# Optimization experiments

Hardware: AMD Instinct MI355X
Metric: run time of the kernel (lower is better)

The kernel has to match this reference:

```python
import jax, jax.numpy as jnp
import numpy as np

IGNORE_LABEL = -1.0
POS_THR, NEG_THR = 0.5, 0.4
BBOX_CLIP = float(np.log(1000.0 / 16.0))


def box_overlap(box, gt):
    # box [M,4], gt [G,4] -> IoU [M,G]  (legacy +1 box widths)
    area_b = (box[:, 2] - box[:, 0] + 1) * (box[:, 3] - box[:, 1] + 1)
    area_g = (gt[:, 2] - gt[:, 0] + 1) * (gt[:, 3] - gt[:, 1] + 1)
    iw = jnp.minimum(box[:, None, 2], gt[None, :, 2]) - jnp.maximum(box[:, None, 0], gt[None, :, 0]) + 1
    ih = jnp.minimum(box[:, None, 3], gt[None, :, 3]) - jnp.maximum(box[:, None, 1], gt[None, :, 1]) + 1
    inter = jnp.maximum(iw, 0.0) * jnp.maximum(ih, 0.0)
    union = area_b[:, None] + area_g[None, :] - inter
    return inter / jnp.maximum(union, 1.0)


def bbox_transform_inv(anchors, deltas):
    # decode deltas [M,4] against anchors [M,4]
    w = anchors[:, 2] - anchors[:, 0] + 1
    h = anchors[:, 3] - anchors[:, 1] + 1
    cx = anchors[:, 0] + 0.5 * w
    cy = anchors[:, 1] + 0.5 * h
    pcx = cx + deltas[:, 0] * w
    pcy = cy + deltas[:, 1] * h
    pw = w * jnp.exp(jnp.minimum(deltas[:, 2], BBOX_CLIP))
    ph = h * jnp.exp(jnp.minimum(deltas[:, 3], BBOX_CLIP))
    return jnp.stack([pcx - 0.5 * pw, pcy - 0.5 * ph, pcx + 0.5 * pw, pcy + 0.5 * ph], axis=1)


def bbox_transform(anchors, gt):
    # encode gt [M,4] against anchors [M,4]
    aw = anchors[:, 2] - anchors[:, 0] + 1
    ah = anchors[:, 3] - anchors[:, 1] + 1
    acx = anchors[:, 0] + 0.5 * aw
    acy = anchors[:, 1] + 0.5 * ah
    gw = gt[:, 2] - gt[:, 0] + 1
    gh = gt[:, 3] - gt[:, 1] + 1
    gcx = gt[:, 0] + 0.5 * gw
    gcy = gt[:, 1] + 0.5 * gh
    return jnp.stack([(gcx - acx) / aw, (gcy - acy) / ah, jnp.log(gw / aw), jnp.log(gh / ah)], axis=1)


def rpn_anchor_target(boxes, anchors4):
    # boxes [n,G,5] -> labels [n,A,2] (top-2 EMD matching), targets [n,2A,4]
    anc2 = jnp.repeat(anchors4, 2, axis=0)  # interleaved [a0,a0,a1,a1,...]
    def per_image(gt):
        ov = box_overlap(anchors4, gt[:, :4])                     # [A,G]
        valid = gt[:, 4] != IGNORE_LABEL
        ov = jnp.where(valid[None, :], ov, -1.0)
        vals, idx = jax.lax.top_k(ov, 2)                          # [A,2]
        labels = jnp.where(vals >= POS_THR, 1.0,
                           jnp.where(vals < NEG_THR, 0.0, IGNORE_LABEL))
        matched = gt[idx.reshape(-1), :4]                         # [2A,4]
        targets = bbox_transform(anc2, matched)
        return labels, targets
    return jax.vmap(per_image)(boxes)


def anchor_iou_target(boxes, anchors4, pred_reg):
    # decode both predictions per anchor, IoU vs gt, then best / 2nd-best match value
    A = anchors4.shape[0]
    anc2 = jnp.repeat(anchors4, 2, axis=0)
    def per_image(gt, off):
        off = off.reshape(-1, 4)                                  # [2A,4]
        dt = bbox_transform_inv(anc2, off)
        ov = box_overlap(dt, gt[:, :4])                           # [2A,G]
        keep = 1.0 - (gt[:, 4] == IGNORE_LABEL).astype(ov.dtype)
        ov = ov * keep[None, :]
        ov = ov.reshape(A, 2, -1)
        a, b = ov[:, 0, :], ov[:, 1, :]
        ia = jnp.argmax(a, axis=1)
        aval = jnp.take_along_axis(a, ia[:, None], axis=1)        # [A,1]
        b = b.at[jnp.arange(A), ia].set(0.0)                      # scatter best slot to 0
        ib = jnp.argmax(b, axis=1)
        bval = jnp.take_along_axis(b, ib[:, None], axis=1)
        return jnp.concatenate([aval, bval], axis=1)              # [A,2]
    return jax.vmap(per_image)(boxes, pred_reg)


def sigmoid_ce_retina(pred, label, alpha=0.25, gamma=2.0):
    # focal loss; pred [n,M,1] probs, label [n,M] in {-1,0,1}
    mask = (label != IGNORE_LABEL).astype(pred.dtype)
    vlabel = label * mask
    onehot = (vlabel == 1.0).astype(pred.dtype)[:, :, None]
    pos = (1.0 - pred) ** gamma * onehot * jnp.log(pred)
    neg = pred ** gamma * (1.0 - onehot) * jnp.log(1.0 - pred)
    loss = -(alpha * pos + (1.0 - alpha) * neg).sum(axis=2) * mask
    npos = jnp.maximum((label > 0).sum(), 1)
    return loss.sum() / npos


def fg_mask(label):
    # label not background(0) and not ignore(-1)
    return ((label != 0.0) & (label != IGNORE_LABEL)).astype(jnp.float32)


def smooth_l1_retina(pred, gt, label, sigma=3.0):
    s2 = sigma * sigma
    x = pred - gt
    ax = jnp.abs(x)
    val = jnp.where(ax < 1.0 / s2, 0.5 * s2 * x * x, ax - 0.5 / s2)
    mask = fg_mask(label)
    return (val.sum(axis=2) * mask).sum() / jnp.maximum(mask.sum(), 1.0)


def iou_l1(pred, target, label):
    mask = fg_mask(label)
    return (jnp.abs(pred - target) * mask).sum() / jnp.maximum(mask.sum(), 1.0)


def softmax_loss_fn(score, label):
    # score [M,c], label [M] ints with -1 = ignore
    logp = jax.nn.log_softmax(score, axis=1)
    mask = label != -1
    vlabel = jnp.where(mask, label, 0).astype(jnp.int32)
    picked = jnp.take_along_axis(logp, vlabel[:, None], axis=1)[:, 0]
    return -(picked * mask).sum() / jnp.maximum(mask.sum(), 1)


def setup_inputs() -> dict:
    key = jax.random.key(0)
    ks = jax.random.split(key, 10)
    n, A, G = 2, 120000, 300
    pred_cls = jax.nn.sigmoid(jax.random.normal(ks[0], (n, A, 2), jnp.float32))
    rpn_num_prob = jax.random.normal(ks[1], (n, A, 2), jnp.float32)
    pred_reg = 0.2 * jax.random.normal(ks[2], (n, A, 8), jnp.float32)
    rpn_iou = jax.nn.sigmoid(jax.random.normal(ks[3], (n, A, 2), jnp.float32))
    cx = jax.random.uniform(ks[4], (A,), minval=0.0, maxval=1024.0)
    cy = jax.random.uniform(ks[5], (A,), minval=0.0, maxval=1024.0)
    w = jax.random.uniform(ks[6], (A,), minval=16.0, maxval=256.0)
    h = jax.random.uniform(ks[7], (A,), minval=16.0, maxval=256.0)
    anchors = jnp.stack([cx - 0.5 * w, cy - 0.5 * h, cx + 0.5 * w, cy + 0.5 * h], axis=1)
    kx, ky, kw, kh, kl = jax.random.split(ks[8], 5)
    gx = jax.random.uniform(kx, (n, G), minval=0.0, maxval=900.0)
    gy = jax.random.uniform(ky, (n, G), minval=0.0, maxval=900.0)
    gw = jax.random.uniform(kw, (n, G), minval=20.0, maxval=200.0)
    gh = jax.random.uniform(kh, (n, G), minval=20.0, maxval=200.0)
    glab = jnp.where(jax.random.uniform(kl, (n, G)) < 0.95, 1.0, -1.0)
    boxes = jnp.stack([gx, gy, gx + gw, gy + gh, glab], axis=2)
    im_info = jnp.concatenate([
        jnp.tile(jnp.array([[1024.0, 1024.0, 1.0, 1024.0, 1024.0]], jnp.float32), (n, 1)),
        jnp.full((n, 1), float(G), jnp.float32)], axis=1)
    return {"pred_cls": pred_cls, "rpn_num_prob": rpn_num_prob, "pred_reg": pred_reg,
            "anchors": anchors, "rpn_iou": rpn_iou, "boxes": boxes, "im_info": im_info}


def reference(pred_cls, rpn_num_prob, pred_reg, anchors, rpn_iou, boxes, im_info):
    n = pred_cls.shape[0]
    anchors4 = anchors[:, :4]
    # anchor targets and iou targets are computed under no_grad in the original
    rpn_labels, rpn_target_boxes = jax.lax.stop_gradient(rpn_anchor_target(boxes, anchors4))
    ious_target = jax.lax.stop_gradient(anchor_iou_target(boxes, anchors4, pred_reg))
    target_boxes = rpn_target_boxes.reshape(n, -1, 4)   # [n,2A,4]
    cls_prob = pred_cls.reshape(n, -1, 1)               # [n,2A,1]
    offsets = pred_reg.reshape(n, -1, 4)                # [n,2A,4]
    a = rpn_labels[:, :, 0]
    b = rpn_labels[:, :, 1]
    ignores = b - (a == 0.0).astype(b.dtype) * (b != 0.0).astype(b.dtype)
    labels = jnp.stack([a, ignores], axis=2).reshape(n, -1)  # [n,2A]
    cls_loss = sigmoid_ce_retina(cls_prob, labels, 0.25, 2.0)
    bbox_loss = smooth_l1_retina(offsets, target_boxes, labels)
    lab2 = labels.reshape(n, -1, 2)
    iou_loss = iou_l1(rpn_iou, ious_target, lab2)
    nlabels = (lab2 > 0).sum(axis=2).reshape(-1).astype(jnp.int32) - 1  # in {-1,0,1}
    num_loss = softmax_loss_fn(rpn_num_prob.reshape(-1, rpn_num_prob.shape[2]), nlabels)
    # order: rpn_cls_loss, rpn_bbox_loss, rpn_iou_loss, rpn_num_loss
    return jnp.stack([cls_loss, 2.0 * bbox_loss, 2.0 * iou_loss, num_loss])
```

## Files before the change

### kernel.cpp

```cpp
#include <hip/hip_runtime.h>
#include <math.h>

#define G_MAX 512
#define SPLIT 4

#define NBIN 264
#define BIN_LO 130.0f
#define BIN_INVW 0.2f

__device__ __forceinline__ float waveSum(float v) {
#pragma unroll
  for (int o = 32; o > 0; o >>= 1) v += __shfl_down(v, o, 64);
  return v;
}

__device__ __forceinline__ float huber9(float x) {
  float ax = fabsf(x);
  return (ax < (1.0f / 9.0f)) ? 4.5f * x * x : ax - (0.5f / 9.0f);
}

__device__ __forceinline__ float iouExact(float bx0, float by0, float bx1, float by1,
                                          float areab, float4 g, float areag) {
  float gx1 = g.z - 1.0f, gy1 = g.w - 1.0f;
  float iw = fminf(bx1, gx1) - fmaxf(bx0, g.x) + 1.0f;
  float ih = fminf(by1, gy1) - fmaxf(by0, g.y) + 1.0f;
  float inter = fmaxf(iw, 0.f) * fmaxf(ih, 0.f);
  float uni = areab + areag - inter;
  return inter / fmaxf(uni, 1.0f);
}

__device__ __forceinline__ uint32_t packKey(float x0, float y0, float x1p, float y1p,
                                            float area, float4 gb, float ga,
                                            uint32_t g) {
  float iw = fminf(x1p, gb.z) - fmaxf(x0, gb.x);
  float ih = fminf(y1p, gb.w) - fmaxf(y0, gb.y);
  float inter = fmaxf(iw, 0.f) * ih;
  float key = (area + ga) * __builtin_amdgcn_rcpf(inter);
  return (__float_as_uint(key) & 0xFFFFFE00u) | g;
}

__device__ __forceinline__ int xbin(float x) {
  return (int)fminf(fmaxf((x + BIN_LO) * BIN_INVW, 0.0f), (float)(NBIN - 1));
}

__global__ __launch_bounds__(256) void retina_main(
    const float* __restrict__ pred_cls,
    const float* __restrict__ rpn_num,
    const float* __restrict__ pred_reg,
    const float* __restrict__ anchors,
    const float* __restrict__ rpn_iou,
    const float* __restrict__ boxes,
    int A, int G,
    double* __restrict__ partial)
{
  __shared__ float4 sBox[G_MAX];
  __shared__ float2 sMeta[G_MAX];
  __shared__ unsigned short sO2S[G_MAX];
  __shared__ int sHist[NBIN];
  __shared__ int sStart[NBIN + 1];
  __shared__ int sCur[NBIN];
  __shared__ float sWaveMax[4];
  __shared__ float sSpanSh;
  __shared__ float sRed[4][7];
  __shared__ float sStash[64][10];
  __shared__ float2 sRes[64];
  __shared__ unsigned char sList[64];
  __shared__ int sNum;

  const int img = blockIdx.y;
  const int seg = threadIdx.x & (SPLIT - 1);
  const int q   = threadIdx.x >> 2;
  const int i   = blockIdx.x * 64 + q;
  const int ic  = (i < A) ? i : (A - 1);
  const float* gtb = boxes + (size_t)img * G * 5;

  float4 a4 = *(const float4*)(anchors + (size_t)ic * 4);
  float ax0 = a4.x, ay0 = a4.y, ax1 = a4.z, ay1 = a4.w;
  float aw = ax1 - ax0 + 1.0f, ah = ay1 - ay0 + 1.0f;
  float areaa = aw * ah;
  float acx = ax0 + 0.5f * aw, acy = ay0 + 0.5f * ah;
  float ax1p = ax1 + 1.0f, ay1p = ay1 + 1.0f;

  float d0 = 0.f, d1 = 0.f, d2 = 0.f, d3 = 0.f;
  float d4 = 0.f, d5 = 0.f, d6 = 0.f, d7 = 0.f;
  float pcv0 = 0.f, pcv1 = 0.f, riv0 = 0.f, riv1 = 0.f, sn0 = 0.f, sn1 = 0.f;
  if (seg == 0) {
    const float* dp = pred_reg + ((size_t)img * A + ic) * 8;
    d0 = dp[0]; d1 = dp[1]; d2 = dp[2]; d3 = dp[3];
    d4 = dp[4]; d5 = dp[5]; d6 = dp[6]; d7 = dp[7];
    const float* pc = pred_cls + ((size_t)img * A + ic) * 2;
    pcv0 = pc[0]; pcv1 = pc[1];
    const float* ri = rpn_iou + ((size_t)img * A + ic) * 2;
    riv0 = ri[0]; riv1 = ri[1];
    const float* sp = rpn_num + ((size_t)img * A + ic) * 2;
    sn0 = sp[0]; sn1 = sp[1];
  }

  if (threadIdx.x == 0) sNum = 0;
  for (int b = threadIdx.x; b < NBIN; b += 256) sHist[b] = 0;
  __syncthreads();

  for (int g = threadIdx.x; g < G; g += 256)
    atomicAdd(&sHist[xbin(gtb[g * 5 + 0])], 1);
  __syncthreads();

  for (int b = threadIdx.x; b <= NBIN; b += 256) {
    int s = 0;
    for (int j = 0; j < b; ++j) s += sHist[j];
    sStart[b] = s;
    if (b < NBIN) sCur[b] = s;
  }
  for (int s = G + threadIdx.x; s < G_MAX; s += 256) {
    sBox[s] = make_float4(0.f, 0.f, 1.f, 1.f);
    sMeta[s] = make_float2(1e30f, __uint_as_float((unsigned)s));
    sO2S[s] = (unsigned short)G;
  }
  __syncthreads();

  float mspan = 0.f;
  for (int g = threadIdx.x; g < G; g += 256) {
    float x0 = gtb[g * 5 + 0], y0 = gtb[g * 5 + 1];
    float x1 = gtb[g * 5 + 2], y1 = gtb[g * 5 + 3];
    float lb = gtb[g * 5 + 4];
    int pos = atomicAdd(&sCur[xbin(x0)], 1);
    float x1p = x1 + 1.0f, y1p = y1 + 1.0f;
    sBox[pos] = make_float4(x0, y0, x1p, y1p);
    sMeta[pos] = make_float2(
        (lb != -1.0f) ? (x1 - x0 + 1.0f) * (y1 - y0 + 1.0f) : 1e30f,
        __uint_as_float((unsigned)g));
    sO2S[g] = (unsigned short)pos;
    mspan = fmaxf(mspan, x1p - x0);
  }
#pragma unroll
  for (int m = 32; m > 0; m >>= 1) mspan = fmaxf(mspan, __shfl_xor(mspan, m, 64));
  {
    int lane = threadIdx.x & 63, wid = threadIdx.x >> 6;
    if (lane == 0) sWaveMax[wid] = mspan;
  }
  __syncthreads();
  if (threadIdx.x == 0)
    sSpanSh = fmaxf(fmaxf(sWaveMax[0], sWaveMax[1]),
                    fmaxf(sWaveMax[2], sWaveMax[3])) + 1.0f;
  __syncthreads();
  const float maxSpan = sSpanSh;

  float t_cls = 0.f, t_bbox = 0.f, t_iou = 0.f, t_num = 0.f;
  float t_npos = 0.f, t_nfg = 0.f, t_ncnt = 0.f;

  const float BBOX_CLIP = 4.1351666f;

  uint32_t an1 = 0xFFFFFFFFu, an2 = 0xFFFFFFFFu;
  {
    int lo = sStart[xbin(ax0 - maxSpan)];
    int hi = sStart[xbin(ax1p) + 1];
#pragma unroll 2
    for (int s = lo + seg; s < hi; s += SPLIT) {
      float4 gb = sBox[s];
      float2 mt = sMeta[s];
      uint32_t pk = packKey(ax0, ay0, ax1p, ay1p, areaa, gb, mt.x,
                            __float_as_uint(mt.y));
      uint32_t h = max(pk, an1);
      an1 = min(an1, pk);
      an2 = min(an2, h);
    }
  }

#pragma unroll
  for (int m = 1; m <= 2; m <<= 1) {
    uint32_t o1 = (uint32_t)__shfl_xor((int)an1, m, 64);
    uint32_t o2 = (uint32_t)__shfl_xor((int)an2, m, 64);
    uint32_t hi = max(an1, o1);
    an1 = min(an1, o1);
    an2 = min(min(an2, o2), hi);
  }

  bool fg0 = false, fg1 = false, needy = false;

  if (seg == 0 && i < A) {
    int og0 = (int)(an1 & 0x1FFu);
    int og1 = (int)(an2 & 0x1FFu);
    int s0 = sO2S[og0];
    int s1 = sO2S[og1];

    float4 g0 = sBox[s0]; float a0 = sMeta[s0].x; bool val0 = a0 < 1e29f;
    float v0 = val0 ? iouExact(ax0, ay0, ax1, ay1, areaa, g0, a0) : -1.0f;
    float4 g1 = sBox[s1]; float a1 = sMeta[s1].x; bool val1 = a1 < 1e29f;
    float v1 = val1 ? iouExact(ax0, ay0, ax1, ay1, areaa, g1, a1) : -1.0f;

    float la  = (v0 >= 0.5f) ? 1.0f : ((v0 < 0.4f) ? 0.0f : -1.0f);
    float lbv = (v1 >= 0.5f) ? 1.0f : ((v1 < 0.4f) ? 0.0f : -1.0f);
    float lab0 = la;
    float lab1 = lbv - (((la == 0.0f) && (lbv != 0.0f)) ? 1.0f : 0.0f);

    {
      float pv = pcv0;
      if (lab0 != -1.0f) {
        float l = (lab0 == 1.0f)
                      ? 0.25f * (1.0f - pv) * (1.0f - pv) * logf(pv)
                      : 0.75f * pv * pv * logf(1.0f - pv);
        t_cls -= l;
      }
      if (lab0 > 0.f) t_npos += 1.f;
      float qv = pcv1;
      if (lab1 != -1.0f) {
        float l = (lab1 == 1.0f)
                      ? 0.25f * (1.0f - qv) * (1.0f - qv) * logf(qv)
                      : 0.75f * qv * qv * logf(1.0f - qv);
        t_cls -= l;
      }
      if (lab1 > 0.f) t_npos += 1.f;
    }

    fg0 = (lab0 != 0.0f) && (lab0 != -1.0f);
    fg1 = (lab1 != 0.0f) && (lab1 != -1.0f);

    float raw = __builtin_amdgcn_rcpf(aw), rah = __builtin_amdgcn_rcpf(ah);

    if (fg0) {
      float mx1 = g0.z - 1.0f, my1 = g0.w - 1.0f;
      float gw = mx1 - g0.x + 1.0f, gh = my1 - g0.y + 1.0f;
      float gcx = g0.x + 0.5f * gw, gcy = g0.y + 0.5f * gh;
      float t0 = (gcx - acx) * raw, t1v = (gcy - acy) * rah;
      float t2 = logf(gw * raw), t3 = logf(gh * rah);
      t_bbox += huber9(d0 - t0) + huber9(d1 - t1v) + huber9(d2 - t2) + huber9(d3 - t3);
      t_nfg += 1.f;
    }
    if (fg1) {
      float mx1 = g1.z - 1.0f, my1 = g1.w - 1.0f;
      float gw = mx1 - g1.x + 1.0f, gh = my1 - g1.y + 1.0f;
      float gcx = g1.x + 0.5f * gw, gcy = g1.y + 0.5f * gh;
      float t0 = (gcx - acx) * raw, t1v = (gcy - acy) * rah;
      float t2 = logf(gw * raw), t3 = logf(gh * rah);
      t_bbox += huber9(d4 - t0) + huber9(d5 - t1v) + huber9(d6 - t2) + huber9(d7 - t3);
      t_nfg += 1.f;
    }

    {
      int nl = ((lab0 > 0.f) ? 1 : 0) + ((lab1 > 0.f) ? 1 : 0) - 1;
      if (nl != -1) {
        float m = fmaxf(sn0, sn1);
        float lse = m + logf(expf(sn0 - m) + expf(sn1 - m));
        float picked = ((nl == 0) ? sn0 : sn1) - lse;
        t_num -= picked;
        t_ncnt += 1.f;
      }
    }

    needy = fg0 || fg1;
    if (needy) {
      float p0cx = acx + d0 * aw, p0cy = acy + d1 * ah;
      float p0w = aw * expf(fminf(d2, BBOX_CLIP));
      float p0h = ah * expf(fminf(d3, BBOX_CLIP));
      float b0x0 = p0cx - 0.5f * p0w, b0y0 = p0cy - 0.5f * p0h;
      float b0x1 = p0cx + 0.5f * p0w, b0y1 = p0cy + 0.5f * p0h;
      float area0 = (b0x1 - b0x0 + 1.0f) * (b0y1 - b0y0 + 1.0f);

      float p1cx = acx + d4 * aw, p1cy = acy + d5 * ah;
      float p1w = aw * expf(fminf(d6, BBOX_CLIP));
      float p1h = ah * expf(fminf(d7, BBOX_CLIP));
      float b1x0 = p1cx - 0.5f * p1w, b1y0 = p1cy - 0.5f * p1h;
      float b1x1 = p1cx + 0.5f * p1w, b1y1 = p1cy + 0.5f * p1h;
      float area1 = (b1x1 - b1x0 + 1.0f) * (b1y1 - b1y0 + 1.0f);

      int slot = atomicAdd(&sNum, 1);
      sList[slot] = (unsigned char)q;
      float* st = sStash[slot];
      st[0] = b0x0; st[1] = b0y0; st[2] = b0x1; st[3] = b0y1; st[4] = area0;
      st[5] = b1x0; st[6] = b1y0; st[7] = b1x1; st[8] = b1y1; st[9] = area1;
    }
  }
  __syncthreads();

  {
    int num = sNum;
    int slot = threadIdx.x >> 2;
    int wseg = threadIdx.x & 3;
    if (slot < num) {
      const float* st = sStash[slot];
      float c0x0 = st[0], c0y0 = st[1], c0x1 = st[2], c0y1 = st[3], car0 = st[4];
      float c1x0 = st[5], c1y0 = st[6], c1x1 = st[7], c1y1 = st[8], car1 = st[9];
      float c0x1p = c0x1 + 1.0f, c0y1p = c0y1 + 1.0f;
      float c1x1p = c1x1 + 1.0f, c1y1p = c1y1 + 1.0f;

      uint32_t am = 0xFFFFFFFFu;
      uint32_t bk1 = 0xFFFFFFFFu, bk2 = 0xFFFFFFFFu;

      int lo = sStart[xbin(fminf(c0x0, c1x0) - maxSpan)];
      int hi = sStart[xbin(fmaxf(c0x1p, c1x1p)) + 1];
#pragma unroll 2
      for (int s = lo + wseg; s < hi; s += 4) {
        float4 gb = sBox[s];
        float2 mt = sMeta[s];
        uint32_t og = __float_as_uint(mt.y);
        am = min(am, packKey(c0x0, c0y0, c0x1p, c0y1p, car0, gb, mt.x, og));
        uint32_t pk = packKey(c1x0, c1y0, c1x1p, c1y1p, car1, gb, mt.x, og);
        uint32_t hib = max(pk, bk1);
        bk1 = min(bk1, pk);
        bk2 = min(bk2, hib);
      }

#pragma unroll
      for (int m = 1; m <= 2; m <<= 1) {
        am = min(am, (uint32_t)__shfl_xor((int)am, m, 64));
        uint32_t q1 = (uint32_t)__shfl_xor((int)bk1, m, 64);
        uint32_t q2 = (uint32_t)__shfl_xor((int)bk2, m, 64);
        uint32_t hib = max(bk1, q1);
        bk1 = min(bk1, q1);
        bk2 = min(min(bk2, q2), hib);
      }

      if (wseg == 0) {
        int ai  = (int)(am  & 0x1FFu);
        int bi  = (int)(bk1 & 0x1FFu);
        int bi2 = (int)(bk2 & 0x1FFu);
        int sa = sO2S[ai];
        float4 ga4 = sBox[sa]; float aav = sMeta[sa].x;
        float aval = (aav < 1e29f) ? iouExact(c0x0, c0y0, c0x1, c0y1, car0, ga4, aav) : 0.0f;
        int bIdx = (ai == bi) ? bi2 : bi;
        int sb = sO2S[bIdx];
        float4 gb4 = sBox[sb]; float abv = sMeta[sb].x;
        float bval = (abv < 1e29f) ? iouExact(c1x0, c1y0, c1x1, c1y1, car1, gb4, abv) : 0.0f;
        sRes[sList[slot]] = make_float2(aval, bval);
      }
    }
  }
  __syncthreads();

  if (needy) {
    float2 r = sRes[q];
    if (fg0) t_iou += fabsf(riv0 - r.x);
    if (fg1) t_iou += fabsf(riv1 - fmaxf(r.y, 0.0f));
  }

  float vals[7] = {t_cls, t_bbox, t_iou, t_num, t_npos, t_nfg, t_ncnt};
  int lane = threadIdx.x & 63;
  int wid = threadIdx.x >> 6;
#pragma unroll
  for (int k = 0; k < 7; ++k) {
    float s = waveSum(vals[k]);
    if (lane == 0) sRed[wid][k] = s;
  }
  __syncthreads();
  if (threadIdx.x < 7) {
    double s = (double)sRed[0][threadIdx.x] + (double)sRed[1][threadIdx.x] +
               (double)sRed[2][threadIdx.x] + (double)sRed[3][threadIdx.x];
    size_t bid = (size_t)blockIdx.y * gridDim.x + blockIdx.x;
    partial[bid * 8 + threadIdx.x] = s;
  }
}

__global__ __launch_bounds__(1024) void retina_finalize(
    const double* __restrict__ partial, int nB, float* __restrict__ out) {
  __shared__ double sRed[16][7];
  double loc[7] = {0.0, 0.0, 0.0, 0.0, 0.0, 0.0, 0.0};
  for (int b = threadIdx.x; b < nB; b += 1024) {
    const double* r = partial + (size_t)b * 8;
#pragma unroll
    for (int k = 0; k < 7; ++k) loc[k] += r[k];
  }
  int lane = threadIdx.x & 63;
  int wid = threadIdx.x >> 6;
#pragma unroll
  for (int k = 0; k < 7; ++k) {
    double v = loc[k];
#pragma unroll
    for (int o = 32; o > 0; o >>= 1) v += __shfl_down(v, o, 64);
    if (lane == 0) sRed[wid][k] = v;
  }
  __syncthreads();
  if (threadIdx.x == 0) {
    double t[7];
#pragma unroll
    for (int k = 0; k < 7; ++k) {
      double s = 0.0;
      for (int w = 0; w < 16; ++w) s += sRed[w][k];
      t[k] = s;
    }
    double dpos = t[4] > 1.0 ? t[4] : 1.0;
    double dfg  = t[5] > 1.0 ? t[5] : 1.0;
    double dcnt = t[6] > 1.0 ? t[6] : 1.0;
    out[0] = (float)(t[0] / dpos);
    out[1] = (float)(2.0 * t[1] / dfg);
    out[2] = (float)(2.0 * t[2] / dfg);
    out[3] = (float)(t[3] / dcnt);
  }
}

extern "C" void kernel_launch(void* const* d_in, const int* in_sizes, int n_in,
                              void* d_out, int out_size, void* d_ws, size_t ws_size,
                              hipStream_t stream) {
  const float* pred_cls = (const float*)d_in[0];
  const float* rpn_num  = (const float*)d_in[1];
  const float* pred_reg = (const float*)d_in[2];
  const float* anchors  = (const float*)d_in[3];
  const float* rpn_iou  = (const float*)d_in[4];
  const float* boxes    = (const float*)d_in[5];

  int A = in_sizes[3] / 4;
  int n = in_sizes[0] / (2 * A);
  int G = in_sizes[5] / (5 * n);

  double* partial = (double*)d_ws;

  int nBx = (A + 63) / 64;
  int nB = nBx * n;
  dim3 grid(nBx, n, 1);
  retina_main<<<grid, dim3(256, 1, 1), 0, stream>>>(
      pred_cls, rpn_num, pred_reg, anchors, rpn_iou, boxes, A, G, partial);
  retina_finalize<<<dim3(1, 1, 1), dim3(1024, 1, 1), 0, stream>>>(
      partial, nB, (float*)d_out);
}
```

Measured before the change: 144.2 us.

## Bin GT boxes on a 2D x/y grid and process 128 anchors per block

Replaces the 1D x-bin histogram with a 64x16 2D grid keyed on box origin, built with a wave-shuffle prefix scan, so each anchor scans only the GT boxes whose bins overlap it in both x and y. Each block now handles 128 anchors with 2 threads per anchor instead of 64 anchors with 4, halving the number of blocks and the per-block GT binning setup. The second matching pass loops over stash batches to cover up to 128 entries. Grid scale constants assume coordinates within about 900, so out-of-range boxes are clamped into edge bins, and the per-row loop adds overhead when the y span is large.

New measurement: 130.5 us. 9.5% less time.

```diff
diff --git a/kernel.cpp b/kernel.cpp
--- a/kernel.cpp
+++ b/kernel.cpp
@@ -2,11 +2,21 @@
 #include <math.h>
 
 #define G_MAX 512
-#define SPLIT 4
-
-#define NBIN 264
-#define BIN_LO 130.0f
-#define BIN_INVW 0.2f
+
+#define XB 64
+#define YB 16
+#define NBINS 1024
+#define SCLX (64.0f / 900.0f)
+#define SCLY (16.0f / 900.0f)
+
+__device__ __forceinline__ int xbin(float v) {
+  int b = (int)(v * SCLX);
+  return min(max(b, 0), XB - 1);
+}
+__device__ __forceinline__ int ybin(float v) {
+  int b = (int)(v * SCLY);
+  return min(max(b, 0), YB - 1);
+}
 
 __device__ __forceinline__ float waveSum(float v) {
 #pragma unroll
@@ -37,10 +47,6 @@
   float inter = fmaxf(iw, 0.f) * ih;
   float key = (area + ga) * __builtin_amdgcn_rcpf(inter);
   return (__float_as_uint(key) & 0xFFFFFE00u) | g;
-}
-
-__device__ __forceinline__ int xbin(float x) {
-  return (int)fminf(fmaxf((x + BIN_LO) * BIN_INVW, 0.0f), (float)(NBIN - 1));
 }
 
 __global__ __launch_bounds__(256) void retina_main(
@@ -56,21 +62,21 @@
   __shared__ float4 sBox[G_MAX];
   __shared__ float2 sMeta[G_MAX];
   __shared__ unsigned short sO2S[G_MAX];
-  __shared__ int sHist[NBIN];
-  __shared__ int sStart[NBIN + 1];
-  __shared__ int sCur[NBIN];
-  __shared__ float sWaveMax[4];
-  __shared__ float sSpanSh;
+  __shared__ int sCnt[NBINS];
+  __shared__ int sStart[NBINS + 1];
+  __shared__ int sWsum[4];
+  __shared__ float sWaveMax[4][2];
+  __shared__ float sSpanX, sSpanY;
   __shared__ float sRed[4][7];
-  __shared__ float sStash[64][10];
-  __shared__ float2 sRes[64];
-  __shared__ unsigned char sList[64];
+  __shared__ float sStash[128][10];
+  __shared__ float2 sRes[128];
+  __shared__ unsigned char sList[128];
   __shared__ int sNum;
 
   const int img = blockIdx.y;
-  const int seg = threadIdx.x & (SPLIT - 1);
-  const int q   = threadIdx.x >> 2;
-  const int i   = blockIdx.x * 64 + q;
+  const int seg = threadIdx.x & 1;
+  const int duo = threadIdx.x >> 1;
+  const int i   = blockIdx.x * 128 + duo;
   const int ic  = (i < A) ? i : (A - 1);
   const float* gtb = boxes + (size_t)img * G * 5;
 
@@ -97,19 +103,7 @@
   }
 
   if (threadIdx.x == 0) sNum = 0;
-  for (int b = threadIdx.x; b < NBIN; b += 256) sHist[b] = 0;
-  __syncthreads();
-
-  for (int g = threadIdx.x; g < G; g += 256)
-    atomicAdd(&sHist[xbin(gtb[g * 5 + 0])], 1);
-  __syncthreads();
-
-  for (int b = threadIdx.x; b <= NBIN; b += 256) {
-    int s = 0;
-    for (int j = 0; j < b; ++j) s += sHist[j];
-    sStart[b] = s;
-    if (b < NBIN) sCur[b] = s;
-  }
+  for (int b = threadIdx.x; b < NBINS; b += 256) sCnt[b] = 0;
   for (int s = G + threadIdx.x; s < G_MAX; s += 256) {
     sBox[s] = make_float4(0.f, 0.f, 1.f, 1.f);
     sMeta[s] = make_float2(1e30f, __uint_as_float((unsigned)s));
@@ -117,32 +111,79 @@
   }
   __syncthreads();
 
-  float mspan = 0.f;
-  for (int g = threadIdx.x; g < G; g += 256) {
-    float x0 = gtb[g * 5 + 0], y0 = gtb[g * 5 + 1];
-    float x1 = gtb[g * 5 + 2], y1 = gtb[g * 5 + 3];
-    float lb = gtb[g * 5 + 4];
-    int pos = atomicAdd(&sCur[xbin(x0)], 1);
-    float x1p = x1 + 1.0f, y1p = y1 + 1.0f;
-    sBox[pos] = make_float4(x0, y0, x1p, y1p);
-    sMeta[pos] = make_float2(
-        (lb != -1.0f) ? (x1 - x0 + 1.0f) * (y1 - y0 + 1.0f) : 1e30f,
-        __uint_as_float((unsigned)g));
-    sO2S[g] = (unsigned short)pos;
-    mspan = fmaxf(mspan, x1p - x0);
-  }
-#pragma unroll
-  for (int m = 32; m > 0; m >>= 1) mspan = fmaxf(mspan, __shfl_xor(mspan, m, 64));
+  float rx0[2], ry0[2], rx1[2], ry1[2], rlb[2];
+  int ng = 0;
+  for (int g = threadIdx.x; g < G; g += 256, ++ng) {
+    rx0[ng] = gtb[g * 5 + 0]; ry0[ng] = gtb[g * 5 + 1];
+    rx1[ng] = gtb[g * 5 + 2]; ry1[ng] = gtb[g * 5 + 3];
+    rlb[ng] = gtb[g * 5 + 4];
+    atomicAdd(&sCnt[(ybin(ry0[ng]) << 6) | xbin(rx0[ng])], 1);
+  }
+  __syncthreads();
+
+  {
+    int t = threadIdx.x;
+    int b0 = sCnt[t * 4 + 0], b1 = sCnt[t * 4 + 1];
+    int b2 = sCnt[t * 4 + 2], b3 = sCnt[t * 4 + 3];
+    int tsum = b0 + b1 + b2 + b3;
+    int lane = t & 63, wid = t >> 6;
+    int incl = tsum;
+#pragma unroll
+    for (int o = 1; o < 64; o <<= 1) {
+      int u = __shfl_up(incl, o, 64);
+      if (lane >= o) incl += u;
+    }
+    if (lane == 63) sWsum[wid] = incl;
+    __syncthreads();
+    int woff = 0;
+    for (int w = 0; w < wid; ++w) woff += sWsum[w];
+    int excl = woff + incl - tsum;
+    sStart[t * 4 + 0] = excl;
+    sStart[t * 4 + 1] = excl + b0;
+    sStart[t * 4 + 2] = excl + b0 + b1;
+    sStart[t * 4 + 3] = excl + b0 + b1 + b2;
+    if (t == 255) sStart[NBINS] = excl + tsum;
+    sCnt[t * 4 + 0] = excl;
+    sCnt[t * 4 + 1] = excl + b0;
+    sCnt[t * 4 + 2] = excl + b0 + b1;
+    sCnt[t * 4 + 3] = excl + b0 + b1 + b2;
+  }
+  __syncthreads();
+
+  float mspanX = 0.f, mspanY = 0.f;
+  {
+    int g = threadIdx.x;
+    for (int k = 0; k < ng; ++k, g += 256) {
+      float x0 = rx0[k], y0 = ry0[k], x1 = rx1[k], y1 = ry1[k], lb = rlb[k];
+      int pos = atomicAdd(&sCnt[(ybin(y0) << 6) | xbin(x0)], 1);
+      float x1p = x1 + 1.0f, y1p = y1 + 1.0f;
+      sBox[pos] = make_float4(x0, y0, x1p, y1p);
+      sMeta[pos] = make_float2(
+          (lb != -1.0f) ? (x1 - x0 + 1.0f) * (y1 - y0 + 1.0f) : 1e30f,
+          __uint_as_float((unsigned)g));
+      sO2S[g] = (unsigned short)pos;
+      mspanX = fmaxf(mspanX, x1p - x0);
+      mspanY = fmaxf(mspanY, y1p - y0);
+    }
+  }
+#pragma unroll
+  for (int m = 32; m > 0; m >>= 1) {
+    mspanX = fmaxf(mspanX, __shfl_xor(mspanX, m, 64));
+    mspanY = fmaxf(mspanY, __shfl_xor(mspanY, m, 64));
+  }
   {
     int lane = threadIdx.x & 63, wid = threadIdx.x >> 6;
-    if (lane == 0) sWaveMax[wid] = mspan;
-  }
-  __syncthreads();
-  if (threadIdx.x == 0)
-    sSpanSh = fmaxf(fmaxf(sWaveMax[0], sWaveMax[1]),
-                    fmaxf(sWaveMax[2], sWaveMax[3])) + 1.0f;
-  __syncthreads();
-  const float maxSpan = sSpanSh;
+    if (lane == 0) { sWaveMax[wid][0] = mspanX; sWaveMax[wid][1] = mspanY; }
+  }
+  __syncthreads();
+  if (threadIdx.x == 0) {
+    sSpanX = fmaxf(fmaxf(sWaveMax[0][0], sWaveMax[1][0]),
+                   fmaxf(sWaveMax[2][0], sWaveMax[3][0])) + 1.0f;
+    sSpanY = fmaxf(fmaxf(sWaveMax[0][1], sWaveMax[1][1]),
+                   fmaxf(sWaveMax[2][1], sWaveMax[3][1])) + 1.0f;
+  }
+  __syncthreads();
+  const float spanX = sSpanX, spanY = sSpanY;
 
   float t_cls = 0.f, t_bbox = 0.f, t_iou = 0.f, t_num = 0.f;
   float t_npos = 0.f, t_nfg = 0.f, t_ncnt = 0.f;
@@ -151,24 +192,29 @@
 
   uint32_t an1 = 0xFFFFFFFFu, an2 = 0xFFFFFFFFu;
   {
-    int lo = sStart[xbin(ax0 - maxSpan)];
-    int hi = sStart[xbin(ax1p) + 1];
+    int xb0 = xbin(ax0 - spanX);
+    int xb1 = xbin(ax1p);
+    int yb0 = ybin(ay0 - spanY);
+    int yb1 = ybin(ay1p);
+    for (int yb = yb0; yb <= yb1; ++yb) {
+      int lo = sStart[(yb << 6) + xb0];
+      int hi = sStart[(yb << 6) + xb1 + 1];
 #pragma unroll 2
-    for (int s = lo + seg; s < hi; s += SPLIT) {
-      float4 gb = sBox[s];
-      float2 mt = sMeta[s];
-      uint32_t pk = packKey(ax0, ay0, ax1p, ay1p, areaa, gb, mt.x,
-                            __float_as_uint(mt.y));
-      uint32_t h = max(pk, an1);
-      an1 = min(an1, pk);
-      an2 = min(an2, h);
-    }
-  }
-
-#pragma unroll
-  for (int m = 1; m <= 2; m <<= 1) {
-    uint32_t o1 = (uint32_t)__shfl_xor((int)an1, m, 64);
-    uint32_t o2 = (uint32_t)__shfl_xor((int)an2, m, 64);
+      for (int s = lo + seg; s < hi; s += 2) {
+        float4 gb = sBox[s];
+        float2 mt = sMeta[s];
+        uint32_t pk = packKey(ax0, ay0, ax1p, ay1p, areaa, gb, mt.x,
+                              __float_as_uint(mt.y));
+        uint32_t h = max(pk, an1);
+        an1 = min(an1, pk);
+        an2 = min(an2, h);
+      }
+    }
+  }
+
+  {
+    uint32_t o1 = (uint32_t)__shfl_xor((int)an1, 1, 64);
+    uint32_t o2 = (uint32_t)__shfl_xor((int)an2, 1, 64);
     uint32_t hi = max(an1, o1);
     an1 = min(an1, o1);
     an2 = min(min(an2, o2), hi);
@@ -263,7 +309,7 @@
       float area1 = (b1x1 - b1x0 + 1.0f) * (b1y1 - b1y0 + 1.0f);
 
       int slot = atomicAdd(&sNum, 1);
-      sList[slot] = (unsigned char)q;
+      sList[slot] = (unsigned char)duo;
       float* st = sStash[slot];
       st[0] = b0x0; st[1] = b0y0; st[2] = b0x1; st[3] = b0y1; st[4] = area0;
       st[5] = b1x0; st[6] = b1y0; st[7] = b1x1; st[8] = b1y1; st[9] = area1;
@@ -273,61 +319,70 @@
 
   {
     int num = sNum;
-    int slot = threadIdx.x >> 2;
-    int wseg = threadIdx.x & 3;
-    if (slot < num) {
-      const float* st = sStash[slot];
-      float c0x0 = st[0], c0y0 = st[1], c0x1 = st[2], c0y1 = st[3], car0 = st[4];
-      float c1x0 = st[5], c1y0 = st[6], c1x1 = st[7], c1y1 = st[8], car1 = st[9];
-      float c0x1p = c0x1 + 1.0f, c0y1p = c0y1 + 1.0f;
-      float c1x1p = c1x1 + 1.0f, c1y1p = c1y1 + 1.0f;
-
-      uint32_t am = 0xFFFFFFFFu;
-      uint32_t bk1 = 0xFFFFFFFFu, bk2 = 0xFFFFFFFFu;
-
-      int lo = sStart[xbin(fminf(c0x0, c1x0) - maxSpan)];
-      int hi = sStart[xbin(fmaxf(c0x1p, c1x1p)) + 1];
+    for (int sb = 0; sb < num; sb += 64) {
+      int slot = sb + (threadIdx.x >> 2);
+      int wseg = threadIdx.x & 3;
+      if (slot < num) {
+        const float* st = sStash[slot];
+        float c0x0 = st[0], c0y0 = st[1], c0x1 = st[2], c0y1 = st[3], car0 = st[4];
+        float c1x0 = st[5], c1y0 = st[6], c1x1 = st[7], c1y1 = st[8], car1 = st[9];
+        float c0x1p = c0x1 + 1.0f, c0y1p = c0y1 + 1.0f;
+        float c1x1p = c1x1 + 1.0f, c1y1p = c1y1 + 1.0f;
+
+        uint32_t am = 0xFFFFFFFFu;
+        uint32_t bk1 = 0xFFFFFFFFu, bk2 = 0xFFFFFFFFu;
+
+        int xb0 = xbin(fminf(c0x0, c1x0) - spanX);
+        int xb1 = xbin(fmaxf(c0x1p, c1x1p));
+        int yb0 = ybin(fminf(c0y0, c1y0) - spanY);
+        int yb1 = ybin(fmaxf(c0y1p, c1y1p));
+        for (int yb = yb0; yb <= yb1; ++yb) {
+          int lo = sStart[(yb << 6) + xb0];
+          int hi = sStart[(yb << 6) + xb1 + 1];
 #pragma unroll 2
-      for (int s = lo + wseg; s < hi; s += 4) {
-        float4 gb = sBox[s];
-        float2 mt = sMeta[s];
-        uint32_t og = __float_as_uint(mt.y);
-        am = min(am, packKey(c0x0, c0y0, c0x1p, c0y1p, car0, gb, mt.x, og));
-        uint32_t pk = packKey(c1x0, c1y0, c1x1p, c1y1p, car1, gb, mt.x, og);
-        uint32_t hib = max(pk, bk1);
-        bk1 = min(bk1, pk);
-        bk2 = min(bk2, hib);
+          for (int s = lo + wseg; s < hi; s += 4) {
+            float4 gb = sBox[s];
+            float2 mt = sMeta[s];
+            uint32_t og = __float_as_uint(mt.y);
+            am = min(am, packKey(c0x0, c0y0, c0x1p, c0y1p, car0, gb, mt.x, og));
+            uint32_t pk = packKey(c1x0, c1y0, c1x1p, c1y1p, car1, gb, mt.x, og);
+            uint32_t hib = max(pk, bk1);
+            bk1 = min(bk1, pk);
+            bk2 = min(min(bk2, hib), bk2);
+            bk2 = min(bk2, hib);
+          }
+        }
+
+#pragma unroll
+        for (int m = 1; m <= 2; m <<= 1) {
+          am = min(am, (uint32_t)__shfl_xor((int)am, m, 64));
+          uint32_t q1 = (uint32_t)__shfl_xor((int)bk1, m, 64);
+          uint32_t q2 = (uint32_t)__shfl_xor((int)bk2, m, 64);
+          uint32_t hib = max(bk1, q1);
+          bk1 = min(bk1, q1);
+          bk2 = min(min(bk2, q2), hib);
+        }
+
+        if (wseg == 0) {
+          int ai  = (int)(am  & 0x1FFu);
+          int bi  = (int)(bk1 & 0x1FFu);
+          int bi2 = (int)(bk2 & 0x1FFu);
+          int sa = sO2S[ai];
+          float4 ga4 = sBox[sa]; float aav = sMeta[sa].x;
+          float aval = (aav < 1e29f) ? iouExact(c0x0, c0y0, c0x1, c0y1, car0, ga4, aav) : 0.0f;
+          int bIdx = (ai == bi) ? bi2 : bi;
+          int sb2 = sO2S[bIdx];
+          float4 gb4 = sBox[sb2]; float abv = sMeta[sb2].x;
+          float bval = (abv < 1e29f) ? iouExact(c1x0, c1y0, c1x1, c1y1, car1, gb4, abv) : 0.0f;
+          sRes[sList[slot]] = make_float2(aval, bval);
+        }
       }
-
-#pragma unroll
-      for (int m = 1; m <= 2; m <<= 1) {
-        am = min(am, (uint32_t)__shfl_xor((int)am, m, 64));
-        uint32_t q1 = (uint32_t)__shfl_xor((int)bk1, m, 64);
-        uint32_t q2 = (uint32_t)__shfl_xor((int)bk2, m, 64);
-        uint32_t hib = max(bk1, q1);
-        bk1 = min(bk1, q1);
-        bk2 = min(min(bk2, q2), hib);
-      }
-
-      if (wseg == 0) {
-        int ai  = (int)(am  & 0x1FFu);
-        int bi  = (int)(bk1 & 0x1FFu);
-        int bi2 = (int)(bk2 & 0x1FFu);
-        int sa = sO2S[ai];
-        float4 ga4 = sBox[sa]; float aav = sMeta[sa].x;
-        float aval = (aav < 1e29f) ? iouExact(c0x0, c0y0, c0x1, c0y1, car0, ga4, aav) : 0.0f;
-        int bIdx = (ai == bi) ? bi2 : bi;
-        int sb = sO2S[bIdx];
-        float4 gb4 = sBox[sb]; float abv = sMeta[sb].x;
-        float bval = (abv < 1e29f) ? iouExact(c1x0, c1y0, c1x1, c1y1, car1, gb4, abv) : 0.0f;
-        sRes[sList[slot]] = make_float2(aval, bval);
-      }
     }
   }
   __syncthreads();
 
   if (needy) {
-    float2 r = sRes[q];
+    float2 r = sRes[duo];
     if (fg0) t_iou += fabsf(riv0 - r.x);
     if (fg1) t_iou += fabsf(riv1 - fmaxf(r.y, 0.0f));
   }
@@ -402,7 +457,7 @@
 
   double* partial = (double*)d_ws;
 
-  int nBx = (A + 63) / 64;
+  int nBx = (A + 127) / 128;
   int nB = nBx * n;
   dim3 grid(nBx, n, 1);
   retina_main<<<grid, dim3(256, 1, 1), 0, stream>>>(
```
